# Kernel optimization log

Hardware: AMD Instinct MI355X
Metric: run time of the kernel (lower is better)

Reference implementation:

```python
import jax, jax.numpy as jnp
import numpy as np

KS = 10       # kernel_size
OUT_N = 10    # pred_frames_num
DCT_N = 10
BN_INV = 1.0 / np.sqrt(1.0 + 1e-5)  # BN eval with running_mean=0, running_var=1


def _get_dct_matrix(N):
    k = np.arange(N)[:, None].astype(np.float64)
    i = np.arange(N)[None, :].astype(np.float64)
    w = np.full((N, 1), np.sqrt(2.0 / N))
    w[0, 0] = np.sqrt(1.0 / N)
    dct_m = w * np.cos(np.pi * (i + 0.5) * k / N)
    idct_m = np.linalg.inv(dct_m)
    return dct_m.astype(np.float32), idct_m.astype(np.float32)


def _conv1d(x, w):
    # x: [B, Cin, L], w: [Cout, Cin, K] -> [B, Cout, L-K+1]
    return jax.lax.conv_general_dilated(x, w, (1,), 'VALID',
                                        dimension_numbers=('NCH', 'OIH', 'NCH'))


def setup_inputs() -> dict:
    keys = iter(jax.random.split(jax.random.key(0), 32))
    def rn(shape, s=0.06):
        return (jax.random.normal(next(keys), shape, jnp.float32) * s)
    d = {}
    d['src'] = jax.random.normal(next(keys), (128, 50, 66), jnp.float32)
    d['convQ_w1'] = rn((256, 66, 6)); d['convQ_w2'] = rn((256, 256, 5))
    d['convK_w1'] = rn((256, 66, 6)); d['convK_w2'] = rn((256, 256, 5))
    d['gc1_w'] = rn((20, 256)); d['gc1_att'] = rn((66, 66)); d['gc1_b'] = rn((256,))
    d['bn1_g'] = 1.0 + rn((16896,), 0.1); d['bn1_b'] = rn((16896,), 0.1)
    d['gcb_w1'] = rn((12, 256, 256)); d['gcb_att1'] = rn((12, 66, 66)); d['gcb_b1'] = rn((12, 256))
    d['gcb_bn1_g'] = 1.0 + rn((12, 16896), 0.1); d['gcb_bn1_b'] = rn((12, 16896), 0.1)
    d['gcb_w2'] = rn((12, 256, 256)); d['gcb_att2'] = rn((12, 66, 66)); d['gcb_b2'] = rn((12, 256))
    d['gcb_bn2_g'] = 1.0 + rn((12, 16896), 0.1); d['gcb_bn2_b'] = rn((12, 16896), 0.1)
    d['gc7_w'] = rn((256, 20)); d['gc7_att'] = rn((66, 66)); d['gc7_b'] = rn((20,))
    return d


def reference(src, convQ_w1, convQ_w2, convK_w1, convK_w2,
              gc1_w, gc1_att, gc1_b, bn1_g, bn1_b,
              gcb_w1, gcb_att1, gcb_b1, gcb_bn1_g, gcb_bn1_b,
              gcb_w2, gcb_att2, gcb_b2, gcb_bn2_g, gcb_bn2_b,
              gc7_w, gc7_att, gc7_b):
    bs, input_n, F = src.shape  # [128, 50, 66]
    dct_np, idct_np = _get_dct_matrix(KS + OUT_N)
    dct_m = jnp.asarray(dct_np)
    idct_m = jnp.asarray(idct_np)

    src_t = jnp.transpose(src, (0, 2, 1))             # [bs, F, T]
    src_key = src_t[:, :, :input_n - OUT_N]           # [bs, F, 40]
    src_query = src_t[:, :, -KS:]                     # [bs, F, 10]

    vn = input_n - KS - OUT_N + 1                     # 31
    vl = KS + OUT_N                                   # 20
    idx = np.arange(vl)[None, :] + np.arange(vn)[:, None]   # [vn, vl]
    src_value = src[:, idx].reshape(bs * vn, vl, F)   # sliding windows
    src_value = jnp.matmul(dct_m[:DCT_N], src_value)  # [bs*vn, 10, F]
    src_value = src_value.reshape(bs, vn, DCT_N, F).transpose(0, 1, 3, 2).reshape(bs, vn, F * DCT_N)

    key = jax.nn.relu(_conv1d(jax.nn.relu(_conv1d(src_key / 1000.0, convK_w1)), convK_w2))    # [bs,256,31]
    query = jax.nn.relu(_conv1d(jax.nn.relu(_conv1d(src_query / 1000.0, convQ_w1)), convQ_w2))  # [bs,256,1]

    score = jnp.matmul(query.transpose(0, 2, 1), key) + 1e-15   # [bs,1,31]
    att = score / jnp.sum(score, axis=2, keepdims=True)
    dct_att = jnp.matmul(att, src_value)[:, 0].reshape(bs, F, DCT_N)  # [bs,66,10]

    idx2 = np.concatenate([np.arange(input_n - KS, input_n), np.full(OUT_N, input_n - 1)])
    input_gcn = src[:, idx2]                                   # [bs,20,66]
    dct_in = jnp.matmul(dct_m[:DCT_N], input_gcn).transpose(0, 2, 1)  # [bs,66,10]
    x = jnp.concatenate([dct_in, dct_att], axis=-1)            # [bs,66,20]

    def gconv(h, A, W, b):
        # support = h @ W ; out = A @ support + b
        return jnp.einsum('nm,bmf->bnf', A, h @ W) + b

    def bn(h, g, b):
        sh = h.shape
        return (h.reshape(sh[0], -1) * (g * BN_INV) + b).reshape(sh)

    y = jnp.tanh(bn(gconv(x, gc1_att, gc1_w, gc1_b), bn1_g, bn1_b))  # [bs,66,256]

    def block(y, p):
        w1, a1, b1, g1, be1, w2, a2, b2, g2, be2 = p
        h = jnp.tanh(bn(gconv(y, a1, w1, b1), g1, be1))
        h = jnp.tanh(bn(gconv(h, a2, w2, b2), g2, be2))
        return h + y, None

    y, _ = jax.lax.scan(block, y, (gcb_w1, gcb_att1, gcb_b1, gcb_bn1_g, gcb_bn1_b,
                                   gcb_w2, gcb_att2, gcb_b2, gcb_bn2_g, gcb_bn2_b))

    y = gconv(y, gc7_att, gc7_w, gc7_b) + x                    # [bs,66,20]
    out_gcn = jnp.matmul(idct_m[:, :DCT_N], y[:, :, :DCT_N].transpose(0, 2, 1))  # [bs,20,66]
    return out_gcn[:, :, None, :]                              # [bs,20,1,66] (itera=1)
```

## Files before the change

### kernel.cpp

```cpp
#include <hip/hip_runtime.h>
#include <hip/hip_bf16.h>


typedef __attribute__((ext_vector_type(8))) short short8;
typedef __attribute__((ext_vector_type(4))) float float4v;
typedef __attribute__((ext_vector_type(4))) unsigned uint4v;

#define BNI 0.9999950000374995f

__device__ __forceinline__ short f2bf(float x){
  unsigned u = __float_as_uint(x);
  unsigned r = (u + 0x7fff + ((u >> 16) & 1)) >> 16;
  return (short)r;
}
__device__ __forceinline__ unsigned pk2(float a, float b){
  return (unsigned)(unsigned short)f2bf(a) | ((unsigned)(unsigned short)f2bf(b) << 16);
}
__device__ __forceinline__ float tanh_f(float x){
  x = fminf(fmaxf(x, -9.f), 9.f);
  float e = __expf(2.f * x);
  return (e - 1.f) * __builtin_amdgcn_rcpf(e + 1.f);
}

__global__ __launch_bounds__(256) void k_prep(
    const float* __restrict__ wK1, const float* __restrict__ wQ1,
    const float* __restrict__ wK2, const float* __restrict__ wQ2,
    const float* __restrict__ gw1, const float* __restrict__ gw2,
    const float* __restrict__ gc1_w,
    const float* __restrict__ g0, const float* __restrict__ be0, const float* __restrict__ b0,
    const float* __restrict__ g1a, const float* __restrict__ be1a, const float* __restrict__ b1a,
    const float* __restrict__ g2a, const float* __restrict__ be2a, const float* __restrict__ b2a,
    float* __restrict__ dct, short* __restrict__ w1T, short* __restrict__ w2T,
    short* __restrict__ wgT, short* __restrict__ gc1wT, unsigned* __restrict__ bnP)
{
  __shared__ short tle[64][72];
  int bid = blockIdx.x, tid = threadIdx.x;
  if (bid < 2){
    int t = bid*256 + tid;
    if (t < 400){
      int k = t / 20, i = t % 20;
      double w = (k == 0) ? sqrt(1.0/20.0) : sqrt(2.0/20.0);
      dct[t] = (float)(w * cos(3.14159265358979323846 * (i + 0.5) * k / 20.0));
    }
  } else if (bid < 1026){
    int idx = (bid-2)*256 + tid;
    int f = idx >> 9, k = idx & 511;
    float v = 0.f;
    if (k < 396){
      int h = k / 66, c = k - h*66;
      const float* s = (f < 256) ? wK1 : wQ1;
      v = s[((f & 255)*66 + c)*6 + h];
    }
    w1T[idx] = f2bf(v);
  } else if (bid < 3586){
    int idx = (bid-1026)*256 + tid;
    int f = idx / 1280, k = idx - f*1280;
    int h = k >> 8, c = k & 255;
    const float* s = (f < 256) ? wK2 : wQ2;
    w2T[idx] = f2bf(s[((f & 255)*256 + c)*5 + h]);
  } else if (bid < 3970){
    int q = bid - 3586;
    int l = q >> 4, sub = q & 15;
    int kt = (sub >> 2)*64, ft = (sub & 3)*64;
    const float* s = (l < 12) ? (gw1 + l*65536) : (gw2 + (l-12)*65536);
    int c = tid & 63, r4 = tid >> 6;
    #pragma unroll
    for (int p = 0; p < 16; p++){
      int k = p*4 + r4;
      tle[k][c] = f2bf(s[(kt + k)*256 + ft + c]);
    }
    __syncthreads();
    #pragma unroll
    for (int p = 0; p < 16; p++){
      int f = p*4 + r4;
      wgT[l*65536 + (ft + f)*256 + kt + c] = tle[c][f];
    }
  } else if (bid < 4002){
    int idx = (bid-3970)*256 + tid;
    int f = idx >> 5, k = idx & 31;
    gc1wT[idx] = f2bf(k < 20 ? gc1_w[k*256 + f] : 0.f);
  } else {
    int idx = (bid-4002)*256 + tid;
    if (idx < 25*16896){
      int li = idx / 16896, r = idx - li*16896;
      int f = r & 255;
      const float *g, *be, *bi;
      if (li == 0){ g = g0; be = be0; bi = b0; }
      else {
        int l = (li - 1) >> 1;
        if (li & 1){ g = g1a + l*16896; be = be1a + l*16896; bi = b1a + l*256; }
        else       { g = g2a + l*16896; be = be2a + l*16896; bi = b2a + l*256; }
      }
      float sc = g[r] * BNI;
      float sh = bi[f] * sc + be[r];
      bnP[idx] = pk2(sc, sh);
    }
  }
}

__global__ __launch_bounds__(256) void k_conv1(const float* __restrict__ src,
    const short* __restrict__ w1T, short* __restrict__ kc1q){
  int b = blockIdx.x, ns = blockIdx.y;
  int f0 = ns*128;
  __shared__ short Aim[48*424];
  __shared__ short Wt[128*72];
  int tid = threadIdx.x;
  for (int idx = tid; idx < 48*424; idx += 256){
    int t = idx / 424, kk = idx - t*424;
    float v = 0.f;
    if (kk < 396 && t < 40){
      int h = kk / 66, c = kk - h*66;
      int row = t + h + ((t >= 35) ? 5 : 0);
      v = src[(b*50 + row)*66 + c] * 1e-3f;
    }
    Aim[idx] = f2bf(v);
  }
  int w = tid >> 6, lane = tid & 63, fl = lane & 15, g = lane >> 4;
  float4v acc[3][2];
  #pragma unroll
  for (int i=0;i<3;i++) for (int n=0;n<2;n++) acc[i][n] = (float4v){0.f,0.f,0.f,0.f};
  for (int kt = 0; kt < 416; kt += 64){
    __syncthreads();
    for (int ch = tid; ch < 128*8; ch += 256){
      int r = ch >> 3, kq = ch & 7;
      *(short8*)&Wt[r*72 + kq*8] = *(const short8*)&w1T[(f0 + r)*512 + kt + kq*8];
    }
    __syncthreads();
    int nst = (416 - kt >= 64) ? 2 : 1;
    for (int s = 0; s < nst; s++){
      int k0 = s*32;
      short8 bfr0 = *(const short8*)&Wt[(w*32 + fl)*72 + k0 + g*8];
      short8 bfr1 = *(const short8*)&Wt[(w*32 + 16 + fl)*72 + k0 + g*8];
      #pragma unroll
      for (int i=0;i<3;i++){
        short8 afr = *(const short8*)&Aim[(i*16 + fl)*424 + kt + k0 + g*8];
        acc[i][0] = __builtin_amdgcn_mfma_f32_16x16x32_bf16(afr, bfr0, acc[i][0], 0,0,0);
        acc[i][1] = __builtin_amdgcn_mfma_f32_16x16x32_bf16(afr, bfr1, acc[i][1], 0,0,0);
      }
    }
  }
  #pragma unroll
  for (int i=0;i<3;i++) for (int n=0;n<2;n++) for (int j=0;j<4;j++){
    int t = i*16 + g*4 + j;
    int f = f0 + w*32 + n*16 + fl;
    float v = fmaxf(acc[i][n][j], 0.f);
    if (t < 35 && f < 256) kc1q[(b*40 + t)*256 + f] = f2bf(v);
    else if (t >= 35 && t < 40 && f >= 256) kc1q[(b*40 + t)*256 + (f - 256)] = f2bf(v);
  }
}

__global__ __launch_bounds__(256) void k_conv2(const short* __restrict__ kc1q,
    const short* __restrict__ w2T, float* __restrict__ key, float* __restrict__ q){
  int b = blockIdx.x, ns = blockIdx.y;
  int f0 = ns*128;
  __shared__ short kcs[40*256];
  __shared__ short Wt[128*136];
  char* kcb = (char*)kcs;
  int tid = threadIdx.x;
  for (int ch = tid; ch < 1280; ch += 256){
    int r = ch >> 5, kq = ch & 31;
    unsigned byte = (unsigned)(r*512 + kq*16) ^ (unsigned)((r & 7) << 4);
    *(short8*)(kcb + byte) = *(const short8*)&kc1q[(b*40 + r)*256 + kq*8];
  }
  int w = tid >> 6, lane = tid & 63, fl = lane & 15, g = lane >> 4;
  float4v acc[2][2];
  #pragma unroll
  for (int i=0;i<2;i++) for (int n=0;n<2;n++) acc[i][n] = (float4v){0.f,0.f,0.f,0.f};
  for (int kt = 0; kt < 1280; kt += 128){
    __syncthreads();
    for (int ch = tid; ch < 128*16; ch += 256){
      int r = ch >> 4, kq = ch & 15;
      *(short8*)&Wt[r*136 + kq*8] = *(const short8*)&w2T[(f0 + r)*1280 + kt + kq*8];
    }
    __syncthreads();
    #pragma unroll
    for (int s = 0; s < 4; s++){
      int k = kt + s*32;
      int h = k >> 8, cb = k & 255;
      short8 bfr0 = *(const short8*)&Wt[(w*32 + fl)*136 + s*32 + g*8];
      short8 bfr1 = *(const short8*)&Wt[(w*32 + 16 + fl)*136 + s*32 + g*8];
      #pragma unroll
      for (int i=0;i<2;i++){
        int t = i*16 + fl;
        int row = t + h + ((t == 31) ? 4 : 0);
        unsigned byte = (unsigned)(row*512 + (cb + g*8)*2) ^ (unsigned)((row & 7) << 4);
        short8 afr = *(const short8*)(kcb + byte);
        acc[i][0] = __builtin_amdgcn_mfma_f32_16x16x32_bf16(afr, bfr0, acc[i][0], 0,0,0);
        acc[i][1] = __builtin_amdgcn_mfma_f32_16x16x32_bf16(afr, bfr1, acc[i][1], 0,0,0);
      }
    }
  }
  #pragma unroll
  for (int i=0;i<2;i++) for (int n=0;n<2;n++) for (int j=0;j<4;j++){
    int t = i*16 + g*4 + j;
    int f = f0 + w*32 + n*16 + fl;
    float v = fmaxf(acc[i][n][j], 0.f);
    if (t < 31 && f < 256) key[(b*31 + t)*256 + f] = v;
    else if (t == 31 && f >= 256) q[b*256 + f - 256] = v;
  }
}

__global__ __launch_bounds__(64) void k_att(const float* __restrict__ q,
    const float* __restrict__ key, float* __restrict__ att){
  int b = blockIdx.x;
  int lane = threadIdx.x;
  float s = 0.f;
  if (lane < 31){
    const float* kr = key + (b*31 + lane)*256;
    const float* qr = q + b*256;
    for (int o = 0; o < 256; o++) s += qr[o] * kr[o];
    s += 1e-15f;
  }
  float tot = s;
  for (int off = 32; off; off >>= 1) tot += __shfl_down(tot, off);
  tot = __shfl(tot, 0);
  if (lane < 31) att[b*32 + lane] = s / tot;
}

__global__ __launch_bounds__(256) void k_build_x(const float* __restrict__ src,
    const float* __restrict__ att, const float* __restrict__ dct,
    float* __restrict__ x, short* __restrict__ x_bf){
  int b = blockIdx.x;
  int tid = threadIdx.x;
  __shared__ float z[20*66];
  __shared__ float a[31];
  for (int i = tid; i < 2560; i += 256) x_bf[b*2560 + i] = 0;
  if (tid < 31) a[tid] = att[b*32 + tid];
  __syncthreads();
  for (int idx = tid; idx < 1320; idx += 256){
    int i = idx / 66, f = idx % 66;
    float s = 0.f;
    for (int v = 0; v < 31; v++) s += a[v] * src[(b*50 + v + i)*66 + f];
    z[idx] = s;
  }
  __syncthreads();
  for (int idx = tid; idx < 660; idx += 256){
    int f = idx / 10, k = idx % 10;
    float s1 = 0.f, s2 = 0.f;
    #pragma unroll
    for (int i = 0; i < 20; i++){
      float d = dct[k*20 + i];
      int tt = (i < 10) ? (40 + i) : 49;
      s1 += d * src[(b*50 + tt)*66 + f];
      s2 += d * z[i*66 + f];
    }
    x[(b*66 + f)*20 + k] = s1;
    x[(b*66 + f)*20 + 10 + k] = s2;
    x_bf[(b*80 + f)*32 + k] = f2bf(s1);
    x_bf[(b*80 + f)*32 + 10 + k] = f2bf(s2);
  }
}


__device__ __forceinline__ void am_addr(int i, const float* __restrict__ Af,
    uint2* u, int* byt){
  int n = i / 24, mq = (i % 24) * 4;
  float v0=0.f, v1=0.f, v2=0.f, v3=0.f;
  if (n < 66){
    if (mq+0 < 66) v0 = Af[n*66 + mq+0];
    if (mq+1 < 66) v1 = Af[n*66 + mq+1];
    if (mq+2 < 66) v2 = Af[n*66 + mq+2];
    if (mq+3 < 66) v3 = Af[n*66 + mq+3];
  }
  u->x = pk2(v0, v1); u->y = pk2(v2, v3);
  *byt = n*256 + ((mq*2) ^ ((n & 15) << 4));
}

__device__ __forceinline__ void stage_Am(const float* __restrict__ Af, int tid,
    char* am_c){
  for (int i = tid; i < 1920; i += 512){
    uint2 u; int byt;
    am_addr(i, Af, &u, &byt);
    *(uint2*)(am_c + byt) = u;
  }
}

template<int KSTEPS, int KSTRIDE, int MODE>
__device__ __forceinline__ void layer_step(
    const short* __restrict__ Wg,
    const unsigned* __restrict__ bnl, const float* __restrict__ Af,
    float4v (&y_r)[2][5], int tid, int w, int fl, int g,
    char* __restrict__ ybf_c, char* __restrict__ tT_c, char* __restrict__ am_c)
{
  const short* wbase = Wg + (w*32 + fl)*KSTRIDE + g*8;
  short8 bw[3][2];
  bw[0][0] = *(const short8*)(wbase);
  bw[0][1] = *(const short8*)(wbase + 16*KSTRIDE);
  if (KSTEPS > 1){
    bw[1][0] = *(const short8*)(wbase + 32);
    bw[1][1] = *(const short8*)(wbase + 16*KSTRIDE + 32);
  }
  uint2 amu[4]; int amb[4];
  #pragma unroll
  for (int s=0;s<4;s++){
    int i = tid + s*512;
    if (i < 1920) am_addr(i, Af, &amu[s], &amb[s]); else amb[s] = -1;
  }

  float4v acc[5][2];
  #pragma unroll
  for (int i=0;i<5;i++){ acc[i][0]=(float4v){0.f,0.f,0.f,0.f}; acc[i][1]=(float4v){0.f,0.f,0.f,0.f}; }
  #pragma unroll
  for (int ks=0; ks<KSTEPS; ks++){
    if (ks + 2 < KSTEPS){
      bw[(ks+2)%3][0] = *(const short8*)(wbase + (ks+2)*32);
      bw[(ks+2)%3][1] = *(const short8*)(wbase + 16*KSTRIDE + (ks+2)*32);
    }
    #pragma unroll
    for (int i=0;i<5;i++){
      int m = i*16 + fl;
      short8 af = *(const short8*)(ybf_c + m*512 + ((ks*64 + g*16) ^ ((m & 15) << 4)));
      acc[i][0] = __builtin_amdgcn_mfma_f32_16x16x32_bf16(af, bw[ks%3][0], acc[i][0], 0,0,0);
      acc[i][1] = __builtin_amdgcn_mfma_f32_16x16x32_bf16(af, bw[ks%3][1], acc[i][1], 0,0,0);
    }
  }
  #pragma unroll
  for (int i=0;i<5;i++){
    int mb = (i*16 + g*4)*2;
    #pragma unroll
    for (int n=0;n<2;n++){
      int f = w*32 + n*16 + fl;
      uint2 u; u.x = pk2(acc[i][n][0], acc[i][n][1]); u.y = pk2(acc[i][n][2], acc[i][n][3]);
      *(uint2*)(tT_c + f*256 + (mb ^ ((f & 15) << 4))) = u;
    }
  }
  #pragma unroll
  for (int s=0;s<4;s++) if (amb[s] >= 0) *(uint2*)(am_c + amb[s]) = amu[s];
  __syncthreads();

  uint4v bnp0[5], bnp1[5];
  #pragma unroll
  for (int n2=0;n2<5;n2++){
    int n = n2*16 + fl; int ns = (n < 66) ? n : 0;
    bnp0[n2] = *(const uint4v*)&bnl[ns*256 + w*32 + g*4];
  }
  float4v a2[2][5];
  #pragma unroll
  for (int i=0;i<2;i++)
    #pragma unroll
    for (int n=0;n<5;n++) a2[i][n] = (float4v){0.f,0.f,0.f,0.f};

#define G2STEP(ks) { \
    short8 bA[5]; \
    _Pragma("unroll") \
    for (int n2=0;n2<5;n2++){ \
      int n = n2*16 + fl; \
      bA[n2] = *(const short8*)(am_c + n*256 + (((ks)*64 + g*16) ^ ((n & 15) << 4))); \
    } \
    _Pragma("unroll") \
    for (int i2=0;i2<2;i2++){ \
      int f = w*32 + i2*16 + fl; \
      short8 af = *(const short8*)(tT_c + f*256 + (((ks)*64 + g*16) ^ ((f & 15) << 4))); \
      _Pragma("unroll") \
      for (int n2=0;n2<5;n2++) \
        a2[i2][n2] = __builtin_amdgcn_mfma_f32_16x16x32_bf16(af, bA[n2], a2[i2][n2], 0,0,0); \
    } }

  G2STEP(0)
  #pragma unroll
  for (int n2=0;n2<5;n2++){
    int n = n2*16 + fl; int ns = (n < 66) ? n : 0;
    bnp1[n2] = *(const uint4v*)&bnl[ns*256 + w*32 + 16 + g*4];
  }
  G2STEP(1)
  G2STEP(2)
#undef G2STEP

  #pragma unroll
  for (int i2=0;i2<2;i2++){
    #pragma unroll
    for (int n2=0;n2<5;n2++){
      int n = n2*16 + fl;
      bool nok = (n < 66);
      float vv[4];
      #pragma unroll
      for (int j=0;j<4;j++){
        unsigned u = (i2 == 0) ? bnp0[n2][j] : bnp1[n2][j];
        float sc = __uint_as_float((u & 0xffffu) << 16);
        float sh = __uint_as_float(u & 0xffff0000u);
        float v = a2[i2][n2][j]*sc + sh;
        v = tanh_f(v);
        if (MODE == 0) y_r[i2][n2][j] = v;
        if (MODE == 2){ v += y_r[i2][n2][j]; y_r[i2][n2][j] = v; }
        vv[j] = nok ? v : 0.f;
      }
      int fb2 = (w*32 + i2*16 + g*4)*2;
      uint2 u2; u2.x = pk2(vv[0], vv[1]); u2.y = pk2(vv[2], vv[3]);
      *(uint2*)(ybf_c + n*512 + (fb2 ^ ((n & 15) << 4))) = u2;
    }
  }
  __syncthreads();
}

__global__ __launch_bounds__(512) void k_mega(const short* __restrict__ x_bf,
    const short* __restrict__ gc1wT, const short* __restrict__ wgT,
    const float* __restrict__ gc1_att,
    const float* __restrict__ a1, const float* __restrict__ a2m,
    const unsigned* __restrict__ bnP,
    const float* __restrict__ gc7_w, const float* __restrict__ gc7_att,
    const float* __restrict__ gc7_b, const float* __restrict__ x,
    const float* __restrict__ dct, float* __restrict__ out)
{
  __shared__ __align__(16) char ybf_c[40960];
  __shared__ __align__(16) char tT_c[65536];
  __shared__ __align__(16) char am_c[20480];
  __shared__ float xo_l[1320];
  __shared__ float dct_l[400];

  int b = blockIdx.x, tid = threadIdx.x;
  int w = tid >> 6, lane = tid & 63, fl = lane & 15, g = lane >> 4;

  for (int i = tid; i < 4096; i += 512) ((float4v*)tT_c)[i] = (float4v){0.f,0.f,0.f,0.f};
  for (int i = tid; i < 400; i += 512) dct_l[i] = dct[i];
  for (int i = tid; i < 320; i += 512){
    int m = i >> 2, kq = i & 3;
    short8 v = *(const short8*)&x_bf[(b*80 + m)*32 + kq*8];
    *(short8*)(ybf_c + m*512 + ((kq*16) ^ ((m & 15) << 4))) = v;
  }
  __syncthreads();

  float4v y_r[2][5];

  layer_step<1,32,0>(gc1wT, bnP, gc1_att, y_r, tid, w, fl, g, ybf_c, tT_c, am_c);
  for (int l = 0; l < 12; l++){
    layer_step<8,256,1>(wgT + l*65536, bnP + (1+2*l)*16896, a1 + l*4356,
                        y_r, tid, w, fl, g, ybf_c, tT_c, am_c);
    layer_step<8,256,2>(wgT + (12+l)*65536, bnP + (2+2*l)*16896, a2m + l*4356,
                        y_r, tid, w, fl, g, ybf_c, tT_c, am_c);
  }

  for (int i = tid; i < 2048; i += 512){
    int f = i >> 6, kq = (i & 63)*4;
    float v0=0.f, v1=0.f, v2=0.f, v3=0.f;
    if (f < 20){
      v0 = gc7_w[(kq+0)*20 + f]; v1 = gc7_w[(kq+1)*20 + f];
      v2 = gc7_w[(kq+2)*20 + f]; v3 = gc7_w[(kq+3)*20 + f];
    }
    uint2 u; u.x = pk2(v0, v1); u.y = pk2(v2, v3);
    *(uint2*)(am_c + f*512 + ((kq*2) ^ ((f & 15) << 4))) = u;
  }
  __syncthreads();

  float4v at[5][2];
  #pragma unroll
  for (int i=0;i<5;i++){ at[i][0] = (float4v){0.f,0.f,0.f,0.f}; at[i][1] = (float4v){0.f,0.f,0.f,0.f}; }
  #pragma unroll
  for (int ks = 0; ks < 8; ks++){
    short8 bf[2];
    #pragma unroll
    for (int n=0;n<2;n++){
      int f = n*16 + fl;
      bf[n] = *(const short8*)(am_c + f*512 + ((ks*64 + g*16) ^ ((f & 15) << 4)));
    }
    #pragma unroll
    for (int i=0;i<5;i++){
      int m = i*16 + fl;
      short8 af = *(const short8*)(ybf_c + m*512 + ((ks*64 + g*16) ^ ((m & 15) << 4)));
      at[i][0] = __builtin_amdgcn_mfma_f32_16x16x32_bf16(af, bf[0], at[i][0], 0,0,0);
      at[i][1] = __builtin_amdgcn_mfma_f32_16x16x32_bf16(af, bf[1], at[i][1], 0,0,0);
    }
  }
  if (w == 0){
    #pragma unroll
    for (int i=0;i<5;i++){
      int mb = (i*16 + g*4)*2;
      #pragma unroll
      for (int n=0;n<2;n++){
        int f = n*16 + fl;
        uint2 u; u.x = pk2(at[i][n][0], at[i][n][1]); u.y = pk2(at[i][n][2], at[i][n][3]);
        *(uint2*)(tT_c + f*256 + (mb ^ ((f & 15) << 4))) = u;
      }
    }
  }
  __syncthreads();
  stage_Am(gc7_att, tid, am_c);
  __syncthreads();

  float4v a2t[2][5];
  #pragma unroll
  for (int i=0;i<2;i++)
    #pragma unroll
    for (int n=0;n<5;n++) a2t[i][n] = (float4v){0.f,0.f,0.f,0.f};
  #pragma unroll
  for (int ks = 0; ks < 3; ks++){
    short8 bA[5];
    #pragma unroll
    for (int n2=0;n2<5;n2++){
      int n = n2*16 + fl;
      bA[n2] = *(const short8*)(am_c + n*256 + ((ks*64 + g*16) ^ ((n & 15) << 4)));
    }
    #pragma unroll
    for (int i2=0;i2<2;i2++){
      int f = i2*16 + fl;
      short8 af = *(const short8*)(tT_c + f*256 + ((ks*64 + g*16) ^ ((f & 15) << 4)));
      #pragma unroll
      for (int n2=0;n2<5;n2++)
        a2t[i2][n2] = __builtin_amdgcn_mfma_f32_16x16x32_bf16(af, bA[n2], a2t[i2][n2], 0,0,0);
    }
  }
  if (w == 0){
    #pragma unroll
    for (int i2=0;i2<2;i2++){
      #pragma unroll
      for (int n2=0;n2<5;n2++){
        int n = n2*16 + fl;
        #pragma unroll
        for (int j=0;j<4;j++){
          int f = i2*16 + g*4 + j;
          if (f < 20 && n < 66)
            xo_l[n*20 + f] = a2t[i2][n2][j] + gc7_b[f] + x[(b*66 + n)*20 + f];
        }
      }
    }
  }
  __syncthreads();

  for (int idx = tid; idx < 1320; idx += 512){
    int r = idx / 66, fn = idx % 66;
    float s = 0.f;
    #pragma unroll
    for (int k = 0; k < 10; k++) s += dct_l[k*20 + r] * xo_l[fn*20 + k];
    out[(b*20 + r)*66 + fn] = s;
  }
}

extern "C" void kernel_launch(void* const* d_in, const int* in_sizes, int n_in,
                              void* d_out, int out_size, void* d_ws, size_t ws_size,
                              hipStream_t stream) {
  const float* src      = (const float*)d_in[0];
  const float* convQ_w1 = (const float*)d_in[1];
  const float* convQ_w2 = (const float*)d_in[2];
  const float* convK_w1 = (const float*)d_in[3];
  const float* convK_w2 = (const float*)d_in[4];
  const float* gc1_w    = (const float*)d_in[5];
  const float* gc1_att  = (const float*)d_in[6];
  const float* gc1_b    = (const float*)d_in[7];
  const float* bn1_g    = (const float*)d_in[8];
  const float* bn1_b    = (const float*)d_in[9];
  const float* gcb_w1   = (const float*)d_in[10];
  const float* gcb_att1 = (const float*)d_in[11];
  const float* gcb_b1   = (const float*)d_in[12];
  const float* gcb_bn1g = (const float*)d_in[13];
  const float* gcb_bn1b = (const float*)d_in[14];
  const float* gcb_w2   = (const float*)d_in[15];
  const float* gcb_att2 = (const float*)d_in[16];
  const float* gcb_b2   = (const float*)d_in[17];
  const float* gcb_bn2g = (const float*)d_in[18];
  const float* gcb_bn2b = (const float*)d_in[19];
  const float* gc7_w    = (const float*)d_in[20];
  const float* gc7_att  = (const float*)d_in[21];
  const float* gc7_b    = (const float*)d_in[22];
  float* out = (float*)d_out;

  float* ws    = (float*)d_ws;
  float* dct   = ws;
  float* x     = ws + 512;
  short* x_bf  = (short*)(ws + 169472);
  short* wgT   = (short*)(ws + 333312);
  short* gc1wT = (short*)(ws + 1119744);
  short* w1T   = (short*)(ws + 1123840);
  short* w2T   = (short*)(ws + 1254912);
  short* kc1q  = (short*)(ws + 1582592);
  float* key   = ws + 2237952;
  float* q     = ws + 3253760;
  float* att   = ws + 3286528;
  unsigned* bnP= (unsigned*)(ws + 3290624);

  k_prep<<<5652, 256, 0, stream>>>(convK_w1, convQ_w1, convK_w2, convQ_w2,
      gcb_w1, gcb_w2, gc1_w,
      bn1_g, bn1_b, gc1_b, gcb_bn1g, gcb_bn1b, gcb_b1,
      gcb_bn2g, gcb_bn2b, gcb_b2,
      dct, w1T, w2T, wgT, gc1wT, bnP);

  k_conv1<<<dim3(128,4), 256, 0, stream>>>(src, w1T, kc1q);
  k_conv2<<<dim3(128,4), 256, 0, stream>>>(kc1q, w2T, key, q);
  k_att<<<128, 64, 0, stream>>>(q, key, att);
  k_build_x<<<128, 256, 0, stream>>>(src, att, dct, x, x_bf);

  k_mega<<<128, 512, 0, stream>>>(x_bf, gc1wT, wgT, gc1_att,
      gcb_att1, gcb_att2, bnP,
      gc7_w, gc7_att, gc7_b, x, dct, out);
}
```

Measured before the change: 304.2 us.

## Preconvert adjacency to bf16 in prep, double-buffer y, fuse attention into build_x

The prep kernel now converts all 26 adjacency matrices into a padded bf16 global layout. Each layer then loads its MFMA B-fragments straight into registers instead of staging through shared memory. This removes one barrier per layer and the per-layer fp32-to-bf16 staging work, and ping-ponging two y buffers avoids a read/write hazard in shared memory. The attention-score kernel is also merged into build_x with a parallel per-row dot product, which saves one launch; the cost is more registers for the 15 preloaded fragments and larger shared memory.

```diff
diff --git a/kernel.cpp b/kernel.cpp
--- a/kernel.cpp
+++ b/kernel.cpp
@@ -27,11 +27,14 @@
     const float* __restrict__ wK2, const float* __restrict__ wQ2,
     const float* __restrict__ gw1, const float* __restrict__ gw2,
     const float* __restrict__ gc1_w,
+    const float* __restrict__ gc1_att, const float* __restrict__ att1,
+    const float* __restrict__ att2, const float* __restrict__ gc7_att,
     const float* __restrict__ g0, const float* __restrict__ be0, const float* __restrict__ b0,
     const float* __restrict__ g1a, const float* __restrict__ be1a, const float* __restrict__ b1a,
     const float* __restrict__ g2a, const float* __restrict__ be2a, const float* __restrict__ b2a,
     float* __restrict__ dct, short* __restrict__ w1T, short* __restrict__ w2T,
-    short* __restrict__ wgT, short* __restrict__ gc1wT, unsigned* __restrict__ bnP)
+    short* __restrict__ wgT, short* __restrict__ gc1wT, short* __restrict__ aG,
+    unsigned* __restrict__ bnP)
 {
   __shared__ short tle[64][72];
   int bid = blockIdx.x, tid = threadIdx.x;
@@ -79,8 +82,18 @@
     int idx = (bid-3970)*256 + tid;
     int f = idx >> 5, k = idx & 31;
     gc1wT[idx] = f2bf(k < 20 ? gc1_w[k*256 + f] : 0.f);
+  } else if (bid < 4782){
+    int idx = (bid-4002)*256 + tid;
+    int li = idx / 7680, r = idx - li*7680;
+    int n = r / 96, m = r - n*96;
+    const float* Af;
+    if (li == 0) Af = gc1_att;
+    else if (li == 25) Af = gc7_att;
+    else if (li & 1) Af = att1 + ((li-1)>>1)*4356;
+    else             Af = att2 + ((li-2)>>1)*4356;
+    aG[idx] = f2bf((n < 66 && m < 66) ? Af[n*66 + m] : 0.f);
   } else {
-    int idx = (bid-4002)*256 + tid;
+    int idx = (bid-4782)*256 + tid;
     if (idx < 25*16896){
       int li = idx / 16896, r = idx - li*16896;
       int f = r & 255;
@@ -200,32 +213,39 @@
   }
 }
 
-__global__ __launch_bounds__(64) void k_att(const float* __restrict__ q,
-    const float* __restrict__ key, float* __restrict__ att){
-  int b = blockIdx.x;
-  int lane = threadIdx.x;
-  float s = 0.f;
-  if (lane < 31){
-    const float* kr = key + (b*31 + lane)*256;
-    const float* qr = q + b*256;
-    for (int o = 0; o < 256; o++) s += qr[o] * kr[o];
-    s += 1e-15f;
-  }
-  float tot = s;
-  for (int off = 32; off; off >>= 1) tot += __shfl_down(tot, off);
-  tot = __shfl(tot, 0);
-  if (lane < 31) att[b*32 + lane] = s / tot;
-}
-
-__global__ __launch_bounds__(256) void k_build_x(const float* __restrict__ src,
-    const float* __restrict__ att, const float* __restrict__ dct,
-    float* __restrict__ x, short* __restrict__ x_bf){
+__global__ __launch_bounds__(256) void k_attx(const float* __restrict__ src,
+    const float* __restrict__ q, const float* __restrict__ key,
+    const float* __restrict__ dct, float* __restrict__ x, short* __restrict__ x_bf){
   int b = blockIdx.x;
   int tid = threadIdx.x;
+  __shared__ float sred[31][9];
+  __shared__ float a[31];
   __shared__ float z[20*66];
-  __shared__ float a[31];
   for (int i = tid; i < 2560; i += 256) x_bf[b*2560 + i] = 0;
-  if (tid < 31) a[tid] = att[b*32 + tid];
+  if (tid < 248){
+    int v = tid >> 3, p = tid & 7;
+    const float* kr = key + (b*31 + v)*256 + p*32;
+    const float* qr = q + b*256 + p*32;
+    float s = 0.f;
+    #pragma unroll
+    for (int o = 0; o < 32; o++) s += qr[o] * kr[o];
+    sred[v][p] = s;
+  }
+  __syncthreads();
+  if (tid < 31){
+    float s = 1e-15f;
+    #pragma unroll
+    for (int p = 0; p < 8; p++) s += sred[tid][p];
+    sred[tid][8] = s;
+  }
+  __syncthreads();
+  if (tid < 64){
+    float v = (tid < 31) ? sred[tid][8] : 0.f;
+    float tot = v;
+    for (int off = 32; off; off >>= 1) tot += __shfl_down(tot, off);
+    tot = __shfl(tot, 0);
+    if (tid < 31) a[tid] = v / tot;
+  }
   __syncthreads();
   for (int idx = tid; idx < 1320; idx += 256){
     int i = idx / 66, f = idx % 66;
@@ -252,35 +272,12 @@
 }
 
 
-__device__ __forceinline__ void am_addr(int i, const float* __restrict__ Af,
-    uint2* u, int* byt){
-  int n = i / 24, mq = (i % 24) * 4;
-  float v0=0.f, v1=0.f, v2=0.f, v3=0.f;
-  if (n < 66){
-    if (mq+0 < 66) v0 = Af[n*66 + mq+0];
-    if (mq+1 < 66) v1 = Af[n*66 + mq+1];
-    if (mq+2 < 66) v2 = Af[n*66 + mq+2];
-    if (mq+3 < 66) v3 = Af[n*66 + mq+3];
-  }
-  u->x = pk2(v0, v1); u->y = pk2(v2, v3);
-  *byt = n*256 + ((mq*2) ^ ((n & 15) << 4));
-}
-
-__device__ __forceinline__ void stage_Am(const float* __restrict__ Af, int tid,
-    char* am_c){
-  for (int i = tid; i < 1920; i += 512){
-    uint2 u; int byt;
-    am_addr(i, Af, &u, &byt);
-    *(uint2*)(am_c + byt) = u;
-  }
-}
-
 template<int KSTEPS, int KSTRIDE, int MODE>
 __device__ __forceinline__ void layer_step(
     const short* __restrict__ Wg,
-    const unsigned* __restrict__ bnl, const float* __restrict__ Af,
-    float4v (&y_r)[2][5], int tid, int w, int fl, int g,
-    char* __restrict__ ybf_c, char* __restrict__ tT_c, char* __restrict__ am_c)
+    const unsigned* __restrict__ bnl, const short* __restrict__ aGl,
+    float4v (&y_r)[2][5], int w, int fl, int g,
+    const char* __restrict__ yin, char* __restrict__ yout, char* __restrict__ tT_c)
 {
   const short* wbase = Wg + (w*32 + fl)*KSTRIDE + g*8;
   short8 bw[3][2];
@@ -290,12 +287,12 @@
     bw[1][0] = *(const short8*)(wbase + 32);
     bw[1][1] = *(const short8*)(wbase + 16*KSTRIDE + 32);
   }
-  uint2 amu[4]; int amb[4];
-  #pragma unroll
-  for (int s=0;s<4;s++){
-    int i = tid + s*512;
-    if (i < 1920) am_addr(i, Af, &amu[s], &amb[s]); else amb[s] = -1;
-  }
+  short8 bA[15];
+  #pragma unroll
+  for (int ks=0;ks<3;ks++)
+    #pragma unroll
+    for (int n2=0;n2<5;n2++)
+      bA[ks*5+n2] = *(const short8*)&aGl[(n2*16 + fl)*96 + ks*32 + g*8];
 
   float4v acc[5][2];
   #pragma unroll
@@ -309,7 +306,7 @@
     #pragma unroll
     for (int i=0;i<5;i++){
       int m = i*16 + fl;
-      short8 af = *(const short8*)(ybf_c + m*512 + ((ks*64 + g*16) ^ ((m & 15) << 4)));
+      short8 af = *(const short8*)(yin + m*512 + ((ks*64 + g*16) ^ ((m & 15) << 4)));
       acc[i][0] = __builtin_amdgcn_mfma_f32_16x16x32_bf16(af, bw[ks%3][0], acc[i][0], 0,0,0);
       acc[i][1] = __builtin_amdgcn_mfma_f32_16x16x32_bf16(af, bw[ks%3][1], acc[i][1], 0,0,0);
     }
@@ -324,9 +321,6 @@
       *(uint2*)(tT_c + f*256 + (mb ^ ((f & 15) << 4))) = u;
     }
   }
-  #pragma unroll
-  for (int s=0;s<4;s++) if (amb[s] >= 0) *(uint2*)(am_c + amb[s]) = amu[s];
-  __syncthreads();
 
   uint4v bnp0[5], bnp1[5];
   #pragma unroll
@@ -341,19 +335,13 @@
     for (int n=0;n<5;n++) a2[i][n] = (float4v){0.f,0.f,0.f,0.f};
 
 #define G2STEP(ks) { \
-    short8 bA[5]; \
-    _Pragma("unroll") \
-    for (int n2=0;n2<5;n2++){ \
-      int n = n2*16 + fl; \
-      bA[n2] = *(const short8*)(am_c + n*256 + (((ks)*64 + g*16) ^ ((n & 15) << 4))); \
-    } \
     _Pragma("unroll") \
     for (int i2=0;i2<2;i2++){ \
       int f = w*32 + i2*16 + fl; \
       short8 af = *(const short8*)(tT_c + f*256 + (((ks)*64 + g*16) ^ ((f & 15) << 4))); \
       _Pragma("unroll") \
       for (int n2=0;n2<5;n2++) \
-        a2[i2][n2] = __builtin_amdgcn_mfma_f32_16x16x32_bf16(af, bA[n2], a2[i2][n2], 0,0,0); \
+        a2[i2][n2] = __builtin_amdgcn_mfma_f32_16x16x32_bf16(af, bA[(ks)*5+n2], a2[i2][n2], 0,0,0); \
     } }
 
   G2STEP(0)
@@ -386,7 +374,7 @@
       }
       int fb2 = (w*32 + i2*16 + g*4)*2;
       uint2 u2; u2.x = pk2(vv[0], vv[1]); u2.y = pk2(vv[2], vv[3]);
-      *(uint2*)(ybf_c + n*512 + (fb2 ^ ((n & 15) << 4))) = u2;
+      *(uint2*)(yout + n*512 + (fb2 ^ ((n & 15) << 4))) = u2;
     }
   }
   __syncthreads();
@@ -394,39 +382,37 @@
 
 __global__ __launch_bounds__(512) void k_mega(const short* __restrict__ x_bf,
     const short* __restrict__ gc1wT, const short* __restrict__ wgT,
-    const float* __restrict__ gc1_att,
-    const float* __restrict__ a1, const float* __restrict__ a2m,
-    const unsigned* __restrict__ bnP,
-    const float* __restrict__ gc7_w, const float* __restrict__ gc7_att,
-    const float* __restrict__ gc7_b, const float* __restrict__ x,
-    const float* __restrict__ dct, float* __restrict__ out)
+    const short* __restrict__ aG, const unsigned* __restrict__ bnP,
+    const float* __restrict__ gc7_w, const float* __restrict__ gc7_b,
+    const float* __restrict__ x, const float* __restrict__ dct,
+    float* __restrict__ out)
 {
-  __shared__ __align__(16) char ybf_c[40960];
+  __shared__ __align__(16) char ybf_c[81920];
   __shared__ __align__(16) char tT_c[65536];
-  __shared__ __align__(16) char am_c[20480];
   __shared__ float xo_l[1320];
   __shared__ float dct_l[400];
 
   int b = blockIdx.x, tid = threadIdx.x;
   int w = tid >> 6, lane = tid & 63, fl = lane & 15, g = lane >> 4;
-
-  for (int i = tid; i < 4096; i += 512) ((float4v*)tT_c)[i] = (float4v){0.f,0.f,0.f,0.f};
+  char* ybf0 = ybf_c;
+  char* ybf1 = ybf_c + 40960;
+
   for (int i = tid; i < 400; i += 512) dct_l[i] = dct[i];
   for (int i = tid; i < 320; i += 512){
     int m = i >> 2, kq = i & 3;
     short8 v = *(const short8*)&x_bf[(b*80 + m)*32 + kq*8];
-    *(short8*)(ybf_c + m*512 + ((kq*16) ^ ((m & 15) << 4))) = v;
+    *(short8*)(ybf0 + m*512 + ((kq*16) ^ ((m & 15) << 4))) = v;
   }
   __syncthreads();
 
   float4v y_r[2][5];
 
-  layer_step<1,32,0>(gc1wT, bnP, gc1_att, y_r, tid, w, fl, g, ybf_c, tT_c, am_c);
+  layer_step<1,32,0>(gc1wT, bnP, aG, y_r, w, fl, g, ybf0, ybf1, tT_c);
   for (int l = 0; l < 12; l++){
-    layer_step<8,256,1>(wgT + l*65536, bnP + (1+2*l)*16896, a1 + l*4356,
-                        y_r, tid, w, fl, g, ybf_c, tT_c, am_c);
-    layer_step<8,256,2>(wgT + (12+l)*65536, bnP + (2+2*l)*16896, a2m + l*4356,
-                        y_r, tid, w, fl, g, ybf_c, tT_c, am_c);
+    layer_step<8,256,1>(wgT + l*65536, bnP + (1+2*l)*16896, aG + (1+2*l)*7680,
+                        y_r, w, fl, g, ybf1, ybf0, tT_c);
+    layer_step<8,256,2>(wgT + (12+l)*65536, bnP + (2+2*l)*16896, aG + (2+2*l)*7680,
+                        y_r, w, fl, g, ybf0, ybf1, tT_c);
   }
 
   for (int i = tid; i < 2048; i += 512){
@@ -437,7 +423,16 @@
       v2 = gc7_w[(kq+2)*20 + f]; v3 = gc7_w[(kq+3)*20 + f];
     }
     uint2 u; u.x = pk2(v0, v1); u.y = pk2(v2, v3);
-    *(uint2*)(am_c + f*512 + ((kq*2) ^ ((f & 15) << 4))) = u;
+    *(uint2*)(ybf0 + f*512 + ((kq*2) ^ ((f & 15) << 4))) = u;
+  }
+  short8 bAt[15];
+  {
+    const short* aGt = aG + 25*7680;
+    #pragma unroll
+    for (int ks=0;ks<3;ks++)
+      #pragma unroll
+      for (int n2=0;n2<5;n2++)
+        bAt[ks*5+n2] = *(const short8*)&aGt[(n2*16 + fl)*96 + ks*32 + g*8];
   }
   __syncthreads();
 
@@ -450,12 +445,12 @@
     #pragma unroll
     for (int n=0;n<2;n++){
       int f = n*16 + fl;
-      bf[n] = *(const short8*)(am_c + f*512 + ((ks*64 + g*16) ^ ((f & 15) << 4)));
+      bf[n] = *(const short8*)(ybf0 + f*512 + ((ks*64 + g*16) ^ ((f & 15) << 4)));
     }
     #pragma unroll
     for (int i=0;i<5;i++){
       int m = i*16 + fl;
-      short8 af = *(const short8*)(ybf_c + m*512 + ((ks*64 + g*16) ^ ((m & 15) << 4)));
+      short8 af = *(const short8*)(ybf1 + m*512 + ((ks*64 + g*16) ^ ((m & 15) << 4)));
       at[i][0] = __builtin_amdgcn_mfma_f32_16x16x32_bf16(af, bf[0], at[i][0], 0,0,0);
       at[i][1] = __builtin_amdgcn_mfma_f32_16x16x32_bf16(af, bf[1], at[i][1], 0,0,0);
     }
@@ -473,8 +468,6 @@
     }
   }
   __syncthreads();
-  stage_Am(gc7_att, tid, am_c);
-  __syncthreads();
 
   float4v a2t[2][5];
   #pragma unroll
@@ -483,19 +476,13 @@
     for (int n=0;n<5;n++) a2t[i][n] = (float4v){0.f,0.f,0.f,0.f};
   #pragma unroll
   for (int ks = 0; ks < 3; ks++){
-    short8 bA[5];
-    #pragma unroll
-    for (int n2=0;n2<5;n2++){
-      int n = n2*16 + fl;
-      bA[n2] = *(const short8*)(am_c + n*256 + ((ks*64 + g*16) ^ ((n & 15) << 4)));
-    }
     #pragma unroll
     for (int i2=0;i2<2;i2++){
       int f = i2*16 + fl;
       short8 af = *(const short8*)(tT_c + f*256 + ((ks*64 + g*16) ^ ((f & 15) << 4)));
       #pragma unroll
       for (int n2=0;n2<5;n2++)
-        a2t[i2][n2] = __builtin_amdgcn_mfma_f32_16x16x32_bf16(af, bA[n2], a2t[i2][n2], 0,0,0);
+        a2t[i2][n2] = __builtin_amdgcn_mfma_f32_16x16x32_bf16(af, bAt[ks*5+n2], a2t[i2][n2], 0,0,0);
     }
   }
   if (w == 0){
@@ -563,21 +550,20 @@
   short* kc1q  = (short*)(ws + 1582592);
   float* key   = ws + 2237952;
   float* q     = ws + 3253760;
-  float* att   = ws + 3286528;
   unsigned* bnP= (unsigned*)(ws + 3290624);
-
-  k_prep<<<5652, 256, 0, stream>>>(convK_w1, convQ_w1, convK_w2, convQ_w2,
+  short* aG    = (short*)(ws + 3713024);
+
+  k_prep<<<6432, 256, 0, stream>>>(convK_w1, convQ_w1, convK_w2, convQ_w2,
       gcb_w1, gcb_w2, gc1_w,
+      gc1_att, gcb_att1, gcb_att2, gc7_att,
       bn1_g, bn1_b, gc1_b, gcb_bn1g, gcb_bn1b, gcb_b1,
       gcb_bn2g, gcb_bn2b, gcb_b2,
-      dct, w1T, w2T, wgT, gc1wT, bnP);
+      dct, w1T, w2T, wgT, gc1wT, aG, bnP);
 
   k_conv1<<<dim3(128,4), 256, 0, stream>>>(src, w1T, kc1q);
   k_conv2<<<dim3(128,4), 256, 0, stream>>>(kc1q, w2T, key, q);
-  k_att<<<128, 64, 0, stream>>>(q, key, att);
-  k_build_x<<<128, 256, 0, stream>>>(src, att, dct, x, x_bf);
-
-  k_mega<<<128, 512, 0, stream>>>(x_bf, gc1wT, wgT, gc1_att,
-      gcb_att1, gcb_att2, bnP,
-      gc7_w, gc7_att, gc7_b, x, dct, out);
-}
+  k_attx<<<128, 256, 0, stream>>>(src, q, key, dct, x, x_bf);
+
+  k_mega<<<128, 512, 0, stream>>>(x_bf, gc1wT, wgT, aG, bnP,
+      gc7_w, gc7_b, x, dct, out);
+}
```

Measured after the change: 328.8 us. 8.1% more time.
